# Performance work log

Hardware: AMD Instinct MI355X
Metric: run time of the kernel (lower is better)

Reference implementation:

```python
import jax, jax.numpy as jnp
import numpy as np

NUM_CLASSES = 80
IMG = 608.0
L_COORD, L_NOOBJ, L_CLS = 5.0, 0.5, 1.0
EPS = 1e-7
ANCHORS = jnp.array([[12,16],[19,36],[40,28],[36,75],[76,55],[72,146],
                     [142,110],[192,243],[459,401]], dtype=jnp.float32).reshape(3, 3, 2)


def _iou(b1, b2):
    # boxes in (cx, cy, w, h); broadcastable shapes [..., 4]
    b1x1 = b1[..., 0] - b1[..., 2] * 0.5; b1y1 = b1[..., 1] - b1[..., 3] * 0.5
    b1x2 = b1[..., 0] + b1[..., 2] * 0.5; b1y2 = b1[..., 1] + b1[..., 3] * 0.5
    b2x1 = b2[..., 0] - b2[..., 2] * 0.5; b2y1 = b2[..., 1] - b2[..., 3] * 0.5
    b2x2 = b2[..., 0] + b2[..., 2] * 0.5; b2y2 = b2[..., 1] + b2[..., 3] * 0.5
    iw = jnp.clip(jnp.minimum(b1x2, b2x2) - jnp.maximum(b1x1, b2x1), 0.0)
    ih = jnp.clip(jnp.minimum(b1y2, b2y2) - jnp.maximum(b1y1, b2y1), 0.0)
    inter = iw * ih
    union = (b1x2 - b1x1) * (b1y2 - b1y1) + (b2x2 - b2x1) * (b2y2 - b2y1) - inter + EPS
    return inter / union


def _scale_loss(pred, anchors, targets):
    # pred: [B, A, H, W, 5+C]; anchors: [A, 2] (pixels); targets: [B, T, 5+C]
    B, A, H, W, _ = pred.shape
    C = pred.shape[-1] - 5
    T = targets.shape[1]

    # ---- decode predictions (decodePredictionsStable) ----
    gy, gx = jnp.meshgrid(jnp.arange(H), jnp.arange(W), indexing='ij')
    grid = jnp.stack([gx, gy], axis=-1).astype(pred.dtype)          # [H, W, 2]
    xy = jax.nn.sigmoid(pred[..., :2])
    wh = jnp.clip(pred[..., 2:4], -10.0, 10.0)
    box_xy = jnp.clip((xy + grid) / jnp.array([W, H], dtype=pred.dtype), 0.0, 1.0)
    box_wh = jnp.clip(jnp.exp(wh) * anchors[None, :, None, None, :] / IMG, 0.0, 1.0)
    pbox = jnp.concatenate([box_xy, box_wh], axis=-1)               # [B,A,H,W,4]
    pconf = jax.nn.sigmoid(pred[..., 4])                            # [B,A,H,W]
    pcls = jax.nn.sigmoid(pred[..., 5:])                            # [B,A,H,W,C]

    # ---- build targets (buildTargetsStable, vectorized scatter) ----
    gtbox = jnp.clip(targets[..., :4], 0.0, 1.0)                    # [B,T,4]
    valid = targets[..., 4] > 0                                     # [B,T]
    gxi = jnp.clip((gtbox[..., 0] * W).astype(jnp.int32), 0, W - 1)
    gyi = jnp.clip((gtbox[..., 1] * H).astype(jnp.int32), 0, H - 1)
    abox = jnp.concatenate([jnp.full((A, 2), 0.5, dtype=pred.dtype), anchors / IMG], axis=-1)
    ious = _iou(abox[None, None, :, :], gtbox[:, :, None, :])       # [B,T,A]
    best = jnp.argmax(ious, axis=-1).astype(jnp.int32)              # first max == torch strict '>' loop
    bidx = jnp.broadcast_to(jnp.arange(B, dtype=jnp.int32)[:, None], (B, T))

    flat = ((bidx * A + best) * H + gyi) * W + gxi                  # [B,T]
    order = jnp.arange(B * T, dtype=jnp.int32).reshape(B, T)
    ncells = B * A * H * W
    winner = jnp.full((ncells,), -1, jnp.int32).at[jnp.where(valid, flat, ncells)].max(order, mode='drop')
    keep = valid & (winner[flat] == order)
    bw = jnp.where(keep, bidx, B)                                   # out-of-range -> dropped

    mask = jnp.zeros((B, A, H, W), pred.dtype).at[bw, best, gyi, gxi].set(1.0, mode='drop')
    tbox = jnp.zeros((B, A, H, W, 4), pred.dtype).at[bw, best, gyi, gxi].set(gtbox, mode='drop')
    tcls = jnp.zeros((B, A, H, W, C), pred.dtype).at[bw, best, gyi, gxi].set(targets[..., 5:5 + C], mode='drop')

    npos = jnp.sum(mask)
    nneg = jnp.asarray(mask.size, pred.dtype) - npos

    # ---- coordinate loss: mean(1 - IoU) over positives ----
    coord = jnp.where(npos > 0, jnp.sum((1.0 - _iou(pbox, tbox)) * mask) / jnp.maximum(npos, 1.0), 0.0)

    # ---- confidence loss: BCE sum/npos + lambdaNoObj * BCE sum/nneg ----
    p = jnp.clip(pconf, 1e-10, 1.0 - 1e-10)
    bce = -(mask * jnp.log(p) + (1.0 - mask) * jnp.log1p(-p))
    conf = jnp.sum(bce * mask) / jnp.maximum(npos, 1.0) \
         + L_NOOBJ * jnp.sum(bce * (1.0 - mask)) / jnp.maximum(nneg, 1.0)

    # ---- class loss: BCE mean over positive rows ----
    pc = jnp.clip(pcls, 1e-10, 1.0 - 1e-10)
    tc = jnp.clip(tcls, 0.0, 1.0)
    bcec = -(tc * jnp.log(pc) + (1.0 - tc) * jnp.log1p(-pc))
    cls = jnp.where(npos > 0, jnp.sum(bcec * mask[..., None]) / jnp.maximum(npos * C, 1.0), 0.0)

    return coord, conf, cls


def setup_inputs() -> dict:
    key = jax.random.key(0)
    k0, k1, k2, k3 = jax.random.split(key, 4)
    B, T, C = 16, 50, NUM_CLASSES
    pred0 = jax.random.normal(k0, (B, 3, 76, 76, 5 + C), dtype=jnp.float32)
    pred1 = jax.random.normal(k1, (B, 3, 38, 38, 5 + C), dtype=jnp.float32)
    pred2 = jax.random.normal(k2, (B, 3, 19, 19, 5 + C), dtype=jnp.float32)
    targets = jax.random.uniform(k3, (B, T, 5 + C), dtype=jnp.float32)
    return {"pred0": pred0, "pred1": pred1, "pred2": pred2, "targets": targets}


def reference(pred0, pred1, pred2, targets):
    coord = jnp.float32(0.0); conf = jnp.float32(0.0); cls = jnp.float32(0.0)
    for s, pred in enumerate((pred0, pred1, pred2)):
        c, cf, cl = _scale_loss(pred, ANCHORS[s], targets)
        coord = coord + c; conf = conf + cf; cls = cls + cl
    total = L_COORD * coord + conf + L_CLS * cls
    return total, coord, conf, cls
```

## Files before the change

### kernel.cpp

```cpp
#include <hip/hip_runtime.h>
#include <math.h>

#define BB   16
#define TT   50
#define BT   (BB*TT)
#define NCLS 80
#define IMGF 608.0f

#define H0 76
#define H1 38
#define H2 19
#define N0 277248
#define N1 69312
#define N2 17328
#define NTOT (N0+N1+N2)

#define F0 5891520
#define F1 1472880
#define F2 368220

#define SB0 1600
#define SB1 400
#define SB2 100
#define NSTREAM (SB0+SB1+SB2)

#define NPOS (3*BT)
#define NPOSBLK (NPOS/4)
#define NBLK (NPOSBLK + NSTREAM)

__constant__ float c_anchors[3][3][2] = {
    {{12.f,16.f},{19.f,36.f},{40.f,28.f}},
    {{36.f,75.f},{76.f,55.f},{72.f,146.f}},
    {{142.f,110.f},{192.f,243.f},{459.f,401.f}}};
__constant__ int c_H[3] = {H0, H1, H2};

__device__ __forceinline__ float sigmoidf_(float x) { return 1.0f / (1.0f + expf(-x)); }
__device__ __forceinline__ float clipf_(float x, float lo, float hi) {
    return fminf(fmaxf(x, lo), hi);
}

__device__ __forceinline__ float iou4(float ax, float ay, float aw, float ah,
                                      float bx, float by, float bw, float bh) {
    float ax1 = ax - aw * 0.5f, ay1 = ay - ah * 0.5f;
    float ax2 = ax + aw * 0.5f, ay2 = ay + ah * 0.5f;
    float bx1 = bx - bw * 0.5f, by1 = by - bh * 0.5f;
    float bx2 = bx + bw * 0.5f, by2 = by + bh * 0.5f;
    float iw = fmaxf(fminf(ax2, bx2) - fmaxf(ax1, bx1), 0.f);
    float ih = fmaxf(fminf(ay2, by2) - fmaxf(ay1, by1), 0.f);
    float inter = iw * ih;
    float uni = (ax2 - ax1) * (ay2 - ay1) + (bx2 - bx1) * (by2 - by1) - inter + 1e-7f;
    return inter / uni;
}

__device__ __forceinline__ int target_cell(const float* tr, int s, float& cx, float& cy,
                                           float& w, float& h, int& best, int& gxi, int& gyi) {
    float t4 = tr[4];
    if (!(t4 > 0.f)) return -1;
    cx = clipf_(tr[0], 0.f, 1.f);
    cy = clipf_(tr[1], 0.f, 1.f);
    w  = clipf_(tr[2], 0.f, 1.f);
    h  = clipf_(tr[3], 0.f, 1.f);
    best = 0;
    float bi = -1e30f;
    #pragma unroll
    for (int a = 0; a < 3; a++) {
        float aw = c_anchors[s][a][0] / IMGF;
        float ah = c_anchors[s][a][1] / IMGF;
        float v = iou4(0.5f, 0.5f, aw, ah, cx, cy, w, h);
        if (v > bi) { bi = v; best = a; }
    }
    int H = c_H[s];
    gxi = (int)(cx * (float)H); gxi = min(max(gxi, 0), H - 1);
    gyi = (int)(cy * (float)H); gyi = min(max(gyi, 0), H - 1);
    return 0;
}

__global__ __launch_bounds__(256) void k_main(const float* __restrict__ p0,
                                              const float* __restrict__ p1,
                                              const float* __restrict__ p2,
                                              const float* __restrict__ targets,
                                              float* __restrict__ noobj_part,
                                              float* __restrict__ pos_part) {
    int blk = blockIdx.x;
    int lane = threadIdx.x & 63;
    int wv = threadIdx.x >> 6;

    if (blk >= NPOSBLK) {
        int sblk = blk - NPOSBLK;
        const float4* p4; unsigned nf4; int local, nb;
        if (sblk < SB0)            { p4 = (const float4*)p0; nf4 = F0; local = sblk;            nb = SB0; }
        else if (sblk < SB0 + SB1) { p4 = (const float4*)p1; nf4 = F1; local = sblk - SB0;      nb = SB1; }
        else                       { p4 = (const float4*)p2; nf4 = F2; local = sblk - SB0 - SB1; nb = SB2; }

        float acc = 0.f;
        unsigned stride = (unsigned)nb * 256u;
        for (unsigned i = (unsigned)local * 256u + threadIdx.x; i < nf4; i += stride) {
            float4 v = p4[i];
            unsigned r = (i * 4u) % 85u;
            if (r >= 1u && r <= 4u) {
                unsigned k = 4u - r;
                float lg = (k == 0u) ? v.x : (k == 1u) ? v.y : (k == 2u) ? v.z : v.w;
                float p = clipf_(sigmoidf_(lg), 1e-10f, 1.0f);
                acc += -log1pf(-p);
            }
        }
        #pragma unroll
        for (int off = 32; off > 0; off >>= 1) acc += __shfl_xor(acc, off, 64);
        __shared__ float sm[4];
        if (lane == 0) sm[wv] = acc;
        __syncthreads();
        if (threadIdx.x == 0)
            noobj_part[sblk] = sm[0] + sm[1] + sm[2] + sm[3];
    } else {
        int item = blk * 4 + wv;
        int s = item / BT;
        int order = item % BT;
        int b = order / TT, t = order % TT;

        float v_coord = 0.f, v_obj = 0.f, v_noadj = 0.f, v_cls = 0.f, v_np = 0.f;

        const float* tr = targets + order * 85;
        float cx, cy, w, h; int best, gxi, gyi;
        if (target_cell(tr, s, cx, cy, w, h, best, gxi, gyi) == 0) {
            int H = c_H[s];
            int flat = ((b * 3 + best) * H + gyi) * H + gxi;

            bool lost = false;
            int tp = t + 1 + lane;
            if (tp < TT) {
                const float* tr2 = targets + (b * TT + tp) * 85;
                float cx2, cy2, w2, h2; int best2, gxi2, gyi2;
                if (target_cell(tr2, s, cx2, cy2, w2, h2, best2, gxi2, gyi2) == 0) {
                    int flat2 = ((b * 3 + best2) * H + gyi2) * H + gxi2;
                    lost = (flat2 == flat);
                }
            }
            if (__ballot(lost) == 0ull) {
                const float* pred = (s == 0) ? p0 : (s == 1) ? p1 : p2;
                const float* pc = pred + (long long)flat * 85;

                float px = sigmoidf_(pc[0]);
                float py = sigmoidf_(pc[1]);
                float bx = clipf_((px + (float)gxi) / (float)H, 0.f, 1.f);
                float by = clipf_((py + (float)gyi) / (float)H, 0.f, 1.f);
                float aw = c_anchors[s][best][0], ah = c_anchors[s][best][1];
                float bwv = clipf_(expf(clipf_(pc[2], -10.f, 10.f)) * aw / IMGF, 0.f, 1.f);
                float bhv = clipf_(expf(clipf_(pc[3], -10.f, 10.f)) * ah / IMGF, 0.f, 1.f);
                float iou = iou4(bx, by, bwv, bhv, cx, cy, w, h);

                float p = clipf_(sigmoidf_(pc[4]), 1e-10f, 1.0f);

                float pcv = clipf_(sigmoidf_(pc[5 + lane]), 1e-10f, 1.0f);
                float tc  = clipf_(tr[5 + lane], 0.f, 1.f);
                float cl  = -(tc * logf(pcv) + (1.f - tc) * log1pf(-pcv));
                if (lane < NCLS - 64) {
                    float pcv2 = clipf_(sigmoidf_(pc[5 + 64 + lane]), 1e-10f, 1.0f);
                    float tc2  = clipf_(tr[5 + 64 + lane], 0.f, 1.f);
                    cl += -(tc2 * logf(pcv2) + (1.f - tc2) * log1pf(-pcv2));
                }
                #pragma unroll
                for (int off = 32; off > 0; off >>= 1) cl += __shfl_xor(cl, off, 64);

                v_coord = 1.f - iou;
                v_obj   = -logf(p);
                v_noadj = -log1pf(-p);
                v_cls   = cl;
                v_np    = 1.f;
            }
        }

        if (lane == 0) {
            float* dst = pos_part + (long long)item * 5;
            dst[0] = v_coord; dst[1] = v_obj; dst[2] = v_noadj;
            dst[3] = v_cls;   dst[4] = v_np;
        }
    }
}

__global__ __launch_bounds__(256) void k_final(const float* __restrict__ noobj_part,
                                               const float* __restrict__ pos_part,
                                               float* __restrict__ out) {
    float nsum[3] = {0.f, 0.f, 0.f};
    for (int i = threadIdx.x; i < NSTREAM; i += 256) {
        float v = noobj_part[i];
        if (i < SB0)            nsum[0] += v;
        else if (i < SB0 + SB1) nsum[1] += v;
        else                    nsum[2] += v;
    }
    float ps[3][5] = {};
    for (int i = threadIdx.x; i < NPOS; i += 256) {
        int s = i / BT;
        #pragma unroll
        for (int q = 0; q < 5; q++) ps[s][q] += pos_part[i * 5 + q];
    }

    __shared__ float red[18][256];
    #pragma unroll
    for (int s = 0; s < 3; s++) {
        red[s][threadIdx.x] = nsum[s];
        #pragma unroll
        for (int q = 0; q < 5; q++) red[3 + s * 5 + q][threadIdx.x] = ps[s][q];
    }
    __syncthreads();
    for (int off = 128; off > 0; off >>= 1) {
        if (threadIdx.x < off) {
            #pragma unroll
            for (int r = 0; r < 18; r++)
                red[r][threadIdx.x] += red[r][threadIdx.x + off];
        }
        __syncthreads();
    }
    if (threadIdx.x == 0) {
        const float ncell[3] = {(float)N0, (float)N1, (float)N2};
        float coord = 0.f, conf = 0.f, cls = 0.f;
        #pragma unroll
        for (int s = 0; s < 3; s++) {
            float noobjTot = red[s][0];
            float co    = red[3 + s * 5 + 0][0];
            float ob    = red[3 + s * 5 + 1][0];
            float noadj = red[3 + s * 5 + 2][0];
            float cl    = red[3 + s * 5 + 3][0];
            float npos  = red[3 + s * 5 + 4][0];
            float nneg = ncell[s] - npos;
            float dn = fmaxf(npos, 1.f);
            conf += ob / dn + 0.5f * (noobjTot - noadj) / fmaxf(nneg, 1.f);
            if (npos > 0.f) {
                coord += co / dn;
                cls   += cl / fmaxf(npos * (float)NCLS, 1.f);
            }
        }
        out[0] = 5.0f * coord + conf + 1.0f * cls;
        out[1] = coord;
        out[2] = conf;
        out[3] = cls;
    }
}

extern "C" void kernel_launch(void* const* d_in, const int* in_sizes, int n_in,
                              void* d_out, int out_size, void* d_ws, size_t ws_size,
                              hipStream_t stream) {
    const float* p0 = (const float*)d_in[0];
    const float* p1 = (const float*)d_in[1];
    const float* p2 = (const float*)d_in[2];
    const float* tg = (const float*)d_in[3];
    float* out = (float*)d_out;

    char* ws = (char*)d_ws;
    float* noobj_part = (float*)ws;
    float* pos_part   = (float*)(ws + 16384);

    k_main<<<NBLK, 256, 0, stream>>>(p0, p1, p2, tg, noobj_part, pos_part);
    k_final<<<1, 256, 0, stream>>>(noobj_part, pos_part, out);
}
```

Measured before the change: 179.2 us.

## Split fused kernel into pos and stream kernels, unroll streaming loads 4x

Splits the combined kernel into a separate positive-target kernel and a streaming no-object reduction kernel, launched back to back on the same stream. The streaming loop now issues four independent float4 loads per iteration to raise memory-level parallelism, and the per-scale block counts are reduced to match the new per-iteration work. This removes the per-block branch between the two roles, at the cost of one extra kernel launch and serialization of the two phases.

```diff
diff --git a/kernel.cpp b/kernel.cpp
--- a/kernel.cpp
+++ b/kernel.cpp
@@ -15,18 +15,17 @@
 #define N2 17328
 #define NTOT (N0+N1+N2)
 
-#define F0 5891520
-#define F1 1472880
-#define F2 368220
-
-#define SB0 1600
-#define SB1 400
-#define SB2 100
+#define F0 5891520u
+#define F1 1472880u
+#define F2 368220u
+
+#define SB0 1440
+#define SB1 360
+#define SB2 90
 #define NSTREAM (SB0+SB1+SB2)
 
 #define NPOS (3*BT)
 #define NPOSBLK (NPOS/4)
-#define NBLK (NPOSBLK + NSTREAM)
 
 __constant__ float c_anchors[3][3][2] = {
     {{12.f,16.f},{19.f,36.f},{40.f,28.f}},
@@ -75,105 +74,121 @@
     return 0;
 }
 
-__global__ __launch_bounds__(256) void k_main(const float* __restrict__ p0,
-                                              const float* __restrict__ p1,
-                                              const float* __restrict__ p2,
-                                              const float* __restrict__ targets,
-                                              float* __restrict__ noobj_part,
-                                              float* __restrict__ pos_part) {
-    int blk = blockIdx.x;
+__device__ __forceinline__ float noobj_of(float4 v, unsigned i) {
+    unsigned r = (i * 4u) % 85u;
+    if (r >= 1u && r <= 4u) {
+        unsigned k = 4u - r;
+        float lg = (k == 0u) ? v.x : (k == 1u) ? v.y : (k == 2u) ? v.z : v.w;
+        float p = clipf_(sigmoidf_(lg), 1e-10f, 1.0f);
+        return -log1pf(-p);
+    }
+    return 0.f;
+}
+
+__global__ __launch_bounds__(256) void k_stream(const float* __restrict__ p0,
+                                                const float* __restrict__ p1,
+                                                const float* __restrict__ p2,
+                                                float* __restrict__ noobj_part) {
+    int sblk = blockIdx.x;
     int lane = threadIdx.x & 63;
     int wv = threadIdx.x >> 6;
 
-    if (blk >= NPOSBLK) {
-        int sblk = blk - NPOSBLK;
-        const float4* p4; unsigned nf4; int local, nb;
-        if (sblk < SB0)            { p4 = (const float4*)p0; nf4 = F0; local = sblk;            nb = SB0; }
-        else if (sblk < SB0 + SB1) { p4 = (const float4*)p1; nf4 = F1; local = sblk - SB0;      nb = SB1; }
-        else                       { p4 = (const float4*)p2; nf4 = F2; local = sblk - SB0 - SB1; nb = SB2; }
-
-        float acc = 0.f;
-        unsigned stride = (unsigned)nb * 256u;
-        for (unsigned i = (unsigned)local * 256u + threadIdx.x; i < nf4; i += stride) {
-            float4 v = p4[i];
-            unsigned r = (i * 4u) % 85u;
-            if (r >= 1u && r <= 4u) {
-                unsigned k = 4u - r;
-                float lg = (k == 0u) ? v.x : (k == 1u) ? v.y : (k == 2u) ? v.z : v.w;
-                float p = clipf_(sigmoidf_(lg), 1e-10f, 1.0f);
-                acc += -log1pf(-p);
+    const float4* p4; unsigned nf4; unsigned local, nb;
+    if (sblk < SB0)            { p4 = (const float4*)p0; nf4 = F0; local = sblk;             nb = SB0; }
+    else if (sblk < SB0 + SB1) { p4 = (const float4*)p1; nf4 = F1; local = sblk - SB0;       nb = SB1; }
+    else                       { p4 = (const float4*)p2; nf4 = F2; local = sblk - SB0 - SB1; nb = SB2; }
+
+    float acc = 0.f;
+    const float4 z = {0.f, 0.f, 0.f, 0.f};
+    for (unsigned base = local * 1024u; base < nf4; base += nb * 1024u) {
+        unsigned i0 = base + threadIdx.x;
+        unsigned i1 = i0 + 256u, i2 = i0 + 512u, i3 = i0 + 768u;
+        float4 v0 = (i0 < nf4) ? p4[i0] : z;
+        float4 v1 = (i1 < nf4) ? p4[i1] : z;
+        float4 v2 = (i2 < nf4) ? p4[i2] : z;
+        float4 v3 = (i3 < nf4) ? p4[i3] : z;
+        acc += noobj_of(v0, i0);
+        acc += noobj_of(v1, i1);
+        acc += noobj_of(v2, i2);
+        acc += noobj_of(v3, i3);
+    }
+    #pragma unroll
+    for (int off = 32; off > 0; off >>= 1) acc += __shfl_xor(acc, off, 64);
+    __shared__ float sm[4];
+    if (lane == 0) sm[wv] = acc;
+    __syncthreads();
+    if (threadIdx.x == 0)
+        noobj_part[sblk] = sm[0] + sm[1] + sm[2] + sm[3];
+}
+
+__global__ __launch_bounds__(256) void k_pos(const float* __restrict__ p0,
+                                             const float* __restrict__ p1,
+                                             const float* __restrict__ p2,
+                                             const float* __restrict__ targets,
+                                             float* __restrict__ pos_part) {
+    int lane = threadIdx.x & 63;
+    int wv = threadIdx.x >> 6;
+    int item = blockIdx.x * 4 + wv;
+    int s = item / BT;
+    int order = item % BT;
+    int b = order / TT, t = order % TT;
+
+    float v_coord = 0.f, v_obj = 0.f, v_noadj = 0.f, v_cls = 0.f, v_np = 0.f;
+
+    const float* tr = targets + order * 85;
+    float cx, cy, w, h; int best, gxi, gyi;
+    if (target_cell(tr, s, cx, cy, w, h, best, gxi, gyi) == 0) {
+        int H = c_H[s];
+        int flat = ((b * 3 + best) * H + gyi) * H + gxi;
+
+        bool lost = false;
+        int tp = t + 1 + lane;
+        if (tp < TT) {
+            const float* tr2 = targets + (b * TT + tp) * 85;
+            float cx2, cy2, w2, h2; int best2, gxi2, gyi2;
+            if (target_cell(tr2, s, cx2, cy2, w2, h2, best2, gxi2, gyi2) == 0) {
+                int flat2 = ((b * 3 + best2) * H + gyi2) * H + gxi2;
+                lost = (flat2 == flat);
             }
         }
-        #pragma unroll
-        for (int off = 32; off > 0; off >>= 1) acc += __shfl_xor(acc, off, 64);
-        __shared__ float sm[4];
-        if (lane == 0) sm[wv] = acc;
-        __syncthreads();
-        if (threadIdx.x == 0)
-            noobj_part[sblk] = sm[0] + sm[1] + sm[2] + sm[3];
-    } else {
-        int item = blk * 4 + wv;
-        int s = item / BT;
-        int order = item % BT;
-        int b = order / TT, t = order % TT;
-
-        float v_coord = 0.f, v_obj = 0.f, v_noadj = 0.f, v_cls = 0.f, v_np = 0.f;
-
-        const float* tr = targets + order * 85;
-        float cx, cy, w, h; int best, gxi, gyi;
-        if (target_cell(tr, s, cx, cy, w, h, best, gxi, gyi) == 0) {
-            int H = c_H[s];
-            int flat = ((b * 3 + best) * H + gyi) * H + gxi;
-
-            bool lost = false;
-            int tp = t + 1 + lane;
-            if (tp < TT) {
-                const float* tr2 = targets + (b * TT + tp) * 85;
-                float cx2, cy2, w2, h2; int best2, gxi2, gyi2;
-                if (target_cell(tr2, s, cx2, cy2, w2, h2, best2, gxi2, gyi2) == 0) {
-                    int flat2 = ((b * 3 + best2) * H + gyi2) * H + gxi2;
-                    lost = (flat2 == flat);
-                }
+        if (__ballot(lost) == 0ull) {
+            const float* pred = (s == 0) ? p0 : (s == 1) ? p1 : p2;
+            const float* pc = pred + (long long)flat * 85;
+
+            float px = sigmoidf_(pc[0]);
+            float py = sigmoidf_(pc[1]);
+            float bx = clipf_((px + (float)gxi) / (float)H, 0.f, 1.f);
+            float by = clipf_((py + (float)gyi) / (float)H, 0.f, 1.f);
+            float aw = c_anchors[s][best][0], ah = c_anchors[s][best][1];
+            float bwv = clipf_(expf(clipf_(pc[2], -10.f, 10.f)) * aw / IMGF, 0.f, 1.f);
+            float bhv = clipf_(expf(clipf_(pc[3], -10.f, 10.f)) * ah / IMGF, 0.f, 1.f);
+            float iou = iou4(bx, by, bwv, bhv, cx, cy, w, h);
+
+            float p = clipf_(sigmoidf_(pc[4]), 1e-10f, 1.0f);
+
+            float pcv = clipf_(sigmoidf_(pc[5 + lane]), 1e-10f, 1.0f);
+            float tc  = clipf_(tr[5 + lane], 0.f, 1.f);
+            float cl  = -(tc * logf(pcv) + (1.f - tc) * log1pf(-pcv));
+            if (lane < NCLS - 64) {
+                float pcv2 = clipf_(sigmoidf_(pc[5 + 64 + lane]), 1e-10f, 1.0f);
+                float tc2  = clipf_(tr[5 + 64 + lane], 0.f, 1.f);
+                cl += -(tc2 * logf(pcv2) + (1.f - tc2) * log1pf(-pcv2));
             }
-            if (__ballot(lost) == 0ull) {
-                const float* pred = (s == 0) ? p0 : (s == 1) ? p1 : p2;
-                const float* pc = pred + (long long)flat * 85;
-
-                float px = sigmoidf_(pc[0]);
-                float py = sigmoidf_(pc[1]);
-                float bx = clipf_((px + (float)gxi) / (float)H, 0.f, 1.f);
-                float by = clipf_((py + (float)gyi) / (float)H, 0.f, 1.f);
-                float aw = c_anchors[s][best][0], ah = c_anchors[s][best][1];
-                float bwv = clipf_(expf(clipf_(pc[2], -10.f, 10.f)) * aw / IMGF, 0.f, 1.f);
-                float bhv = clipf_(expf(clipf_(pc[3], -10.f, 10.f)) * ah / IMGF, 0.f, 1.f);
-                float iou = iou4(bx, by, bwv, bhv, cx, cy, w, h);
-
-                float p = clipf_(sigmoidf_(pc[4]), 1e-10f, 1.0f);
-
-                float pcv = clipf_(sigmoidf_(pc[5 + lane]), 1e-10f, 1.0f);
-                float tc  = clipf_(tr[5 + lane], 0.f, 1.f);
-                float cl  = -(tc * logf(pcv) + (1.f - tc) * log1pf(-pcv));
-                if (lane < NCLS - 64) {
-                    float pcv2 = clipf_(sigmoidf_(pc[5 + 64 + lane]), 1e-10f, 1.0f);
-                    float tc2  = clipf_(tr[5 + 64 + lane], 0.f, 1.f);
-                    cl += -(tc2 * logf(pcv2) + (1.f - tc2) * log1pf(-pcv2));
-                }
-                #pragma unroll
-                for (int off = 32; off > 0; off >>= 1) cl += __shfl_xor(cl, off, 64);
-
-                v_coord = 1.f - iou;
-                v_obj   = -logf(p);
-                v_noadj = -log1pf(-p);
-                v_cls   = cl;
-                v_np    = 1.f;
-            }
-        }
-
-        if (lane == 0) {
-            float* dst = pos_part + (long long)item * 5;
-            dst[0] = v_coord; dst[1] = v_obj; dst[2] = v_noadj;
-            dst[3] = v_cls;   dst[4] = v_np;
-        }
+            #pragma unroll
+            for (int off = 32; off > 0; off >>= 1) cl += __shfl_xor(cl, off, 64);
+
+            v_coord = 1.f - iou;
+            v_obj   = -logf(p);
+            v_noadj = -log1pf(-p);
+            v_cls   = cl;
+            v_np    = 1.f;
+        }
+    }
+
+    if (lane == 0) {
+        float* dst = pos_part + (long long)item * 5;
+        dst[0] = v_coord; dst[1] = v_obj; dst[2] = v_noadj;
+        dst[3] = v_cls;   dst[4] = v_np;
     }
 }
 
@@ -249,6 +264,7 @@
     float* noobj_part = (float*)ws;
     float* pos_part   = (float*)(ws + 16384);
 
-    k_main<<<NBLK, 256, 0, stream>>>(p0, p1, p2, tg, noobj_part, pos_part);
+    k_pos<<<NPOSBLK, 256, 0, stream>>>(p0, p1, p2, tg, pos_part);
+    k_stream<<<NSTREAM, 256, 0, stream>>>(p0, p1, p2, noobj_part);
     k_final<<<1, 256, 0, stream>>>(noobj_part, pos_part, out);
 }
```

Measured after the change: 189.8 us. +5.9%, slower.
